# Performance work log

Measured on AMD Instinct MI355X. Metric: run time of the kernel, lower is better.

The kernel has to match this reference:

```python
import jax, jax.numpy as jnp
import numpy as np

SOFTCAP = 30.0  # final_logit_softcapping (Gemma2)


def setup_inputs() -> dict:
    key = jax.random.key(0)
    ks = jax.random.split(key, 6)
    B, S, D, V = 32, 8, 2048, 128000
    return {
        "embedding": jax.random.normal(ks[0], (V, D), jnp.float32) * 0.02,
        "hidden_states": jax.random.normal(ks[1], (B, S, D), jnp.float32),
        "temperatures": jax.random.uniform(ks[2], (B,), jnp.float32, 0.5, 1.0),
        "top_ps": jax.random.uniform(ks[3], (B,), jnp.float32, 0.5, 1.0),
        "output_positions": jax.random.randint(ks[4], (1,), 0, S),
        "top_ks": jax.random.randint(ks[5], (B,), 1, 64),
    }


def reference(embedding, hidden_states, temperatures, top_ps, output_positions, top_ks):
    # select decode position: [B, 1, D] -> [B, D]
    hs = jnp.take(hidden_states, output_positions, axis=1).squeeze(1)
    # logits over vocab: [B, V]
    logits = jnp.einsum("bd,vd->bv", hs, embedding)
    # final logit softcapping
    logits = jnp.tanh(logits / SOFTCAP) * SOFTCAP
    # temperature scaling (matches in-place div; returned logits are scaled)
    logits = logits / temperatures[:, None]
    probs = jax.nn.softmax(logits.astype(jnp.float32), axis=-1)
    # sort descending
    idx = jnp.argsort(-probs, axis=-1)                      # [B, V]
    probs_sort = jnp.take_along_axis(probs, idx, axis=-1)   # [B, V]
    cum = jnp.cumsum(probs_sort, axis=-1)
    V = probs.shape[-1]
    mask = ((cum - probs_sort) > top_ps[:, None]) | (
        jnp.arange(V)[None, :] >= top_ks[:, None]
    )
    probs_sort = jnp.where(mask, 0.0, probs_sort)
    probs_sort = probs_sort / probs_sort.sum(axis=-1, keepdims=True)
    # scatter back to vocab order
    inv = jnp.argsort(idx, axis=-1)
    probs_final = jnp.take_along_axis(probs_sort, inv, axis=-1)
    # multinomial sample (one draw per row)
    next_token_ids = jax.random.categorical(
        jax.random.key(42), jnp.log(probs_final), axis=-1
    )
    return next_token_ids, logits
```

## Files before the change

### kernel.cpp

```cpp
#include <hip/hip_runtime.h>
#include <float.h>
#include <math.h>

#define VOCAB 128000
#define DIM   2048
#define SEQL  8
#define NB    32
#define SCAP  4096

__device__ __forceinline__ unsigned f2sortable(float x){
  unsigned u = __float_as_uint(x);
  return (u & 0x80000000u) ? ~u : (u | 0x80000000u);
}
__device__ __forceinline__ unsigned rotl32(unsigned x, int d){
  return (x << d) | (x >> (32 - d));
}

__device__ float jax_gumbel(unsigned n){
  unsigned x0 = 0u, x1 = n;
  const unsigned k0 = 0u, k1 = 42u;
  const unsigned k2 = 0x1BD11BDAu ^ k0 ^ k1;
  x0 += k0; x1 += k1;
#define TFR(r) { x0 += x1; x1 = rotl32(x1, r); x1 ^= x0; }
  TFR(13) TFR(15) TFR(26) TFR(6)
  x0 += k1; x1 += k2 + 1u;
  TFR(17) TFR(29) TFR(16) TFR(24)
  x0 += k2; x1 += k0 + 2u;
  TFR(13) TFR(15) TFR(26) TFR(6)
  x0 += k0; x1 += k1 + 3u;
  TFR(17) TFR(29) TFR(16) TFR(24)
  x0 += k1; x1 += k2 + 4u;
  TFR(13) TFR(15) TFR(26) TFR(6)
  x0 += k2; x1 += k0 + 5u;
#undef TFR
  unsigned bits = x0 ^ x1;
  float f = __uint_as_float((bits >> 9) | 0x3f800000u) - 1.0f;
  float u = f + 1.17549435e-38f;
  return -logf(-logf(u));
}

__global__ __launch_bounds__(256) void k_logits(
    const float* __restrict__ E, const float* __restrict__ HS,
    const float* __restrict__ temps, const int* __restrict__ posp,
    float* __restrict__ C)
{
  __shared__ float hs_s[2][NB * 64];
  __shared__ float tile[NB * 32];
  const int tid  = threadIdx.x;
  const int w    = tid >> 6;
  const int lane = tid & 63;
  const int g    = lane >> 4;
  const int qi   = lane & 15;
  const int pos  = posp[0];
  const int vbase = blockIdx.x * 32;
  const int vw    = vbase + w * 8;

  float acc[8][8];
#pragma unroll
  for (int j = 0; j < 8; ++j)
#pragma unroll
    for (int bl = 0; bl < 8; ++bl) acc[j][bl] = 0.f;

  const int sb0 = w * 8 + g;
  const int sb1 = w * 8 + 4 + g;
  const float* hsp0 = HS + ((size_t)(sb0 * SEQL + pos)) * DIM + qi * 4;
  const float* hsp1 = HS + ((size_t)(sb1 * SEQL + pos)) * DIM + qi * 4;
  const int lo0 = sb0 * 64 + qi * 4;
  const int lo1 = sb1 * 64 + qi * 4;

  {
    float4 a = *(const float4*)hsp0;
    float4 c = *(const float4*)hsp1;
    *(float4*)&hs_s[0][lo0] = a;
    *(float4*)&hs_s[0][lo1] = c;
  }

  const float* Eb = E + (size_t)vw * DIM + qi * 4;

  for (int s = 0; s < 32; ++s){
    __syncthreads();
    float4 e[8];
#pragma unroll
    for (int j = 0; j < 8; ++j)
      e[j] = *(const float4*)(Eb + (size_t)j * DIM + s * 64);
    float4 n0, n1;
    const bool more = (s + 1 < 32);
    if (more){
      n0 = *(const float4*)(hsp0 + (s + 1) * 64);
      n1 = *(const float4*)(hsp1 + (s + 1) * 64);
    }
    const float* hb = &hs_s[s & 1][0];
#pragma unroll
    for (int bl = 0; bl < 8; ++bl){
      float4 h = *(const float4*)(hb + (g * 8 + bl) * 64 + qi * 4);
#pragma unroll
      for (int j = 0; j < 8; ++j){
        acc[j][bl] = fmaf(e[j].x, h.x, acc[j][bl]);
        acc[j][bl] = fmaf(e[j].y, h.y, acc[j][bl]);
        acc[j][bl] = fmaf(e[j].z, h.z, acc[j][bl]);
        acc[j][bl] = fmaf(e[j].w, h.w, acc[j][bl]);
      }
    }
    if (more){
      float* wb = &hs_s[(s + 1) & 1][0];
      *(float4*)&wb[lo0] = n0;
      *(float4*)&wb[lo1] = n1;
    }
  }

#pragma unroll
  for (int j = 0; j < 8; ++j)
#pragma unroll
    for (int bl = 0; bl < 8; ++bl){
      float v = acc[j][bl];
      v += __shfl_xor(v, 1, 64);
      v += __shfl_xor(v, 2, 64);
      v += __shfl_xor(v, 4, 64);
      v += __shfl_xor(v, 8, 64);
      acc[j][bl] = v;
    }
  if (qi == 0){
#pragma unroll
    for (int j = 0; j < 8; ++j)
#pragma unroll
      for (int bl = 0; bl < 8; ++bl)
        tile[(g * 8 + bl) * 32 + w * 8 + j] = acc[j][bl];
  }
  __syncthreads();
  {
    const int b = tid >> 3, vq = tid & 7;
    const float tmp = temps[b];
    float4 tv = *(const float4*)&tile[b * 32 + vq * 4];
    float4 o;
    o.x = (tanhf(tv.x / 30.f) * 30.f) / tmp;
    o.y = (tanhf(tv.y / 30.f) * 30.f) / tmp;
    o.z = (tanhf(tv.z / 30.f) * 30.f) / tmp;
    o.w = (tanhf(tv.w / 30.f) * 30.f) / tmp;
    *(float4*)(C + (size_t)b * VOCAB + vbase + vq * 4) = o;
  }
}

__global__ __launch_bounds__(1024) void k_sample_fused(
    const float* __restrict__ C,
    const float* __restrict__ tps, const int* __restrict__ tks,
    float* __restrict__ out_tok)
{
  const int b = blockIdx.x, t = threadIdx.x;
  const float* row = C + (size_t)b * VOCAB;
  __shared__ float red[1024];
  __shared__ unsigned ps[1024];
  __shared__ unsigned hist[4096];
  __shared__ float    cval_s[SCAP];
  __shared__ int      cidx_s[SCAP];
  __shared__ int tbin_s;
  __shared__ unsigned cnt_s;

  if (t == 0) cnt_s = 0u;

  float m = -FLT_MAX;
  for (int f = t; f < VOCAB / 4; f += 1024){
    float4 x = ((const float4*)row)[f];
    m = fmaxf(m, fmaxf(fmaxf(x.x, x.y), fmaxf(x.z, x.w)));
  }
  red[t] = m; __syncthreads();
  for (int sft = 512; sft > 0; sft >>= 1){
    if (t < sft) red[t] = fmaxf(red[t], red[t + sft]);
    __syncthreads();
  }
  m = red[0];
  for (int i = t; i < 4096; i += 1024) hist[i] = 0u;
  __syncthreads();

  float zs = 0.f;
  for (int f = t; f < VOCAB / 4; f += 1024){
    float4 x4 = ((const float4*)row)[f];
    float xs[4] = {x4.x, x4.y, x4.z, x4.w};
#pragma unroll
    for (int c = 0; c < 4; ++c){
      zs += expf(xs[c] - m);
      atomicAdd(&hist[f2sortable(xs[c]) >> 20], 1u);
    }
  }
  red[t] = zs; __syncthreads();
  for (int sft = 512; sft > 0; sft >>= 1){
    if (t < sft) red[t] += red[t + sft];
    __syncthreads();
  }
  const float Z = red[0];

  unsigned s_t = 0u;
#pragma unroll
  for (int k = 0; k < 4; ++k) s_t += hist[t * 4 + k];
  ps[t] = s_t; __syncthreads();
  for (int off = 1; off < 1024; off <<= 1){
    unsigned v = ps[t] + ((t + off < 1024) ? ps[t + off] : 0u);
    __syncthreads();
    ps[t] = v;
    __syncthreads();
  }
  const unsigned Sstrict = ps[t] - s_t;
  if (Sstrict < 64u && ps[t] >= 64u){
    unsigned c = Sstrict;
    for (int bb = 3; bb >= 0; --bb){
      c += hist[t * 4 + bb];
      if (c >= 64u){ tbin_s = t * 4 + bb; break; }
    }
  }
  __syncthreads();
  const unsigned thr = ((unsigned)tbin_s) << 20;

  for (int f = t; f < VOCAB / 4; f += 1024){
    float4 x4 = ((const float4*)row)[f];
    float xs[4] = {x4.x, x4.y, x4.z, x4.w};
#pragma unroll
    for (int c = 0; c < 4; ++c){
      if (f2sortable(xs[c]) >= thr){
        unsigned slot = atomicAdd(&cnt_s, 1u);
        if (slot < (unsigned)SCAP){
          cval_s[slot] = xs[c];
          cidx_s[slot] = f * 4 + c;
        }
      }
    }
  }
  __syncthreads();
  int cn = (int)cnt_s; if (cn > SCAP) cn = SCAP;

  for (int j = t; j < cn; j += 1024)
    cval_s[j] = expf(cval_s[j] - m) / Z;
  __syncthreads();

  if (t < 64){
    float my_sp = 0.f; int my_si = 0;
    float lp = FLT_MAX; int li = -1;
    for (int r = 0; r < 64; ++r){
      float bp = -1.f; int bi = 0x7fffffff;
      for (int j = t; j < cn; j += 64){
        float p = cval_s[j]; int id = cidx_s[j];
        bool valid = (p < lp) || (p == lp && id > li);
        if (valid && (p > bp || (p == bp && id < bi))){ bp = p; bi = id; }
      }
#pragma unroll
      for (int off = 32; off >= 1; off >>= 1){
        float op = __shfl_xor(bp, off, 64);
        int   oi = __shfl_xor(bi, off, 64);
        if (op > bp || (op == bp && oi < bi)){ bp = op; bi = oi; }
      }
      if (t == r){ my_sp = bp; my_si = bi; }
      lp = bp; li = bi;
    }

    const float tp = tps[b];
    const int   tk = tks[b];
    float c = 0.f, sren = 0.f;
    bool keep_me = false;
    for (int j = 0; j < 64; ++j){
      float pj = __shfl(my_sp, j, 64);
      c = c + pj;
      float excl = c - pj;
      bool keep = (!(excl > tp)) && (j < tk);
      if (j == t) keep_me = keep;
      if (keep) sren = sren + pj;
    }

    float score = -FLT_MAX;
    int vid = my_si;
    if (keep_me){
      float pf = my_sp / sren;
      score = logf(pf) + jax_gumbel((unsigned)(b * VOCAB + vid));
    }
    float bs = score; int bv = vid;
#pragma unroll
    for (int off = 32; off >= 1; off >>= 1){
      float os = __shfl_xor(bs, off, 64);
      int   ov = __shfl_xor(bv, off, 64);
      if (os > bs || (os == bs && ov < bv)){ bs = os; bv = ov; }
    }
    if (t == 0) out_tok[b] = (float)bv;
  }
}

extern "C" void kernel_launch(void* const* d_in, const int* in_sizes, int n_in,
                              void* d_out, int out_size, void* d_ws, size_t ws_size,
                              hipStream_t stream)
{
  (void)in_sizes; (void)n_in; (void)out_size; (void)d_ws; (void)ws_size;
  const float* emb   = (const float*)d_in[0];
  const float* hs    = (const float*)d_in[1];
  const float* temps = (const float*)d_in[2];
  const float* tps   = (const float*)d_in[3];
  const int*   posp  = (const int*)d_in[4];
  const int*   tks   = (const int*)d_in[5];
  float* out = (float*)d_out;
  float* C   = out + NB;

  k_logits      <<<dim3(VOCAB / 32), dim3(256),  0, stream>>>(emb, hs, temps, posp, C);
  k_sample_fused<<<dim3(NB),         dim3(1024), 0, stream>>>(C, tps, tks, out);
}
```

Measured before the change: 477.6 us.

## Split logits GEMV over four D-slices with full hidden-state LDS preload

The logits kernel now processes one 512-wide slice of the hidden dimension per launch, with four launches accumulating partial dot products into the output buffer. Each launch loads that slice of all batch hidden states into shared memory once, removing the per-step double buffering and block barriers. In exchange, the intermediate logits are read and written multiple times through global memory. The larger shared-memory footprint may also lower occupancy, and the extra launches add overhead.

```diff
diff --git a/kernel.cpp b/kernel.cpp
--- a/kernel.cpp
+++ b/kernel.cpp
@@ -7,6 +7,7 @@
 #define SEQL  8
 #define NB    32
 #define SCAP  4096
+#define QD    512
 
 __device__ __forceinline__ unsigned f2sortable(float x){
   unsigned u = __float_as_uint(x);
@@ -39,13 +40,13 @@
   return -logf(-logf(u));
 }
 
-__global__ __launch_bounds__(256) void k_logits(
+__global__ __launch_bounds__(256) void k_logits_part(
     const float* __restrict__ E, const float* __restrict__ HS,
     const float* __restrict__ temps, const int* __restrict__ posp,
-    float* __restrict__ C)
+    float* __restrict__ C, int q, int first, int last)
 {
-  __shared__ float hs_s[2][NB * 64];
-  __shared__ float tile[NB * 32];
+  __shared__ float hs_s[NB * QD];
+  __shared__ float tile[NB * NB];
   const int tid  = threadIdx.x;
   const int w    = tid >> 6;
   const int lane = tid & 63;
@@ -54,6 +55,16 @@
   const int pos  = posp[0];
   const int vbase = blockIdx.x * 32;
   const int vw    = vbase + w * 8;
+  const int qd0   = q * QD;
+
+#pragma unroll
+  for (int k = 0; k < 16; ++k){
+    const int ff = tid + k * 256;
+    const int b  = ff >> 7;
+    const int d4 = ff & 127;
+    float4 v = *(const float4*)(HS + ((size_t)(b * SEQL + pos)) * DIM + qd0 + d4 * 4);
+    *(float4*)&hs_s[ff * 4] = v;
+  }
 
   float acc[8][8];
 #pragma unroll
@@ -61,38 +72,19 @@
 #pragma unroll
     for (int bl = 0; bl < 8; ++bl) acc[j][bl] = 0.f;
 
-  const int sb0 = w * 8 + g;
-  const int sb1 = w * 8 + 4 + g;
-  const float* hsp0 = HS + ((size_t)(sb0 * SEQL + pos)) * DIM + qi * 4;
-  const float* hsp1 = HS + ((size_t)(sb1 * SEQL + pos)) * DIM + qi * 4;
-  const int lo0 = sb0 * 64 + qi * 4;
-  const int lo1 = sb1 * 64 + qi * 4;
-
-  {
-    float4 a = *(const float4*)hsp0;
-    float4 c = *(const float4*)hsp1;
-    *(float4*)&hs_s[0][lo0] = a;
-    *(float4*)&hs_s[0][lo1] = c;
-  }
-
-  const float* Eb = E + (size_t)vw * DIM + qi * 4;
-
-  for (int s = 0; s < 32; ++s){
-    __syncthreads();
+  __syncthreads();
+
+  const float* Eb = E + (size_t)vw * DIM + qd0 + qi * 4;
+
+  for (int s = 0; s < 8; ++s){
     float4 e[8];
 #pragma unroll
     for (int j = 0; j < 8; ++j)
       e[j] = *(const float4*)(Eb + (size_t)j * DIM + s * 64);
-    float4 n0, n1;
-    const bool more = (s + 1 < 32);
-    if (more){
-      n0 = *(const float4*)(hsp0 + (s + 1) * 64);
-      n1 = *(const float4*)(hsp1 + (s + 1) * 64);
-    }
-    const float* hb = &hs_s[s & 1][0];
+    const float* hb = &hs_s[0];
 #pragma unroll
     for (int bl = 0; bl < 8; ++bl){
-      float4 h = *(const float4*)(hb + (g * 8 + bl) * 64 + qi * 4);
+      float4 h = *(const float4*)(hb + (g * 8 + bl) * QD + s * 64 + qi * 4);
 #pragma unroll
       for (int j = 0; j < 8; ++j){
         acc[j][bl] = fmaf(e[j].x, h.x, acc[j][bl]);
@@ -100,11 +92,6 @@
         acc[j][bl] = fmaf(e[j].z, h.z, acc[j][bl]);
         acc[j][bl] = fmaf(e[j].w, h.w, acc[j][bl]);
       }
-    }
-    if (more){
-      float* wb = &hs_s[(s + 1) & 1][0];
-      *(float4*)&wb[lo0] = n0;
-      *(float4*)&wb[lo1] = n1;
     }
   }
 
@@ -129,14 +116,20 @@
   __syncthreads();
   {
     const int b = tid >> 3, vq = tid & 7;
-    const float tmp = temps[b];
+    float* cp = C + (size_t)b * VOCAB + vbase + vq * 4;
     float4 tv = *(const float4*)&tile[b * 32 + vq * 4];
-    float4 o;
-    o.x = (tanhf(tv.x / 30.f) * 30.f) / tmp;
-    o.y = (tanhf(tv.y / 30.f) * 30.f) / tmp;
-    o.z = (tanhf(tv.z / 30.f) * 30.f) / tmp;
-    o.w = (tanhf(tv.w / 30.f) * 30.f) / tmp;
-    *(float4*)(C + (size_t)b * VOCAB + vbase + vq * 4) = o;
+    if (!first){
+      float4 prev = *(const float4*)cp;
+      tv.x += prev.x; tv.y += prev.y; tv.z += prev.z; tv.w += prev.w;
+    }
+    if (last){
+      const float tmp = temps[b];
+      tv.x = (tanhf(tv.x / 30.f) * 30.f) / tmp;
+      tv.y = (tanhf(tv.y / 30.f) * 30.f) / tmp;
+      tv.z = (tanhf(tv.z / 30.f) * 30.f) / tmp;
+      tv.w = (tanhf(tv.w / 30.f) * 30.f) / tmp;
+    }
+    *(float4*)cp = tv;
   }
 }
 
@@ -294,6 +287,8 @@
   float* out = (float*)d_out;
   float* C   = out + NB;
 
-  k_logits      <<<dim3(VOCAB / 32), dim3(256),  0, stream>>>(emb, hs, temps, posp, C);
-  k_sample_fused<<<dim3(NB),         dim3(1024), 0, stream>>>(C, tps, tks, out);
-}
+  for (int q = 0; q < 4; ++q)
+    k_logits_part<<<dim3(VOCAB / 32), dim3(256), 0, stream>>>(
+        emb, hs, temps, posp, C, q, q == 0 ? 1 : 0, q == 3 ? 1 : 0);
+  k_sample_fused<<<dim3(NB), dim3(1024), 0, stream>>>(C, tps, tks, out);
+}
```

Result: slower. 604.6 us (+26.6%).
